# Kernel tuning notes

Measured on AMD Instinct MI355X. Metric: run time of the kernel, lower is better.

The kernel has to match this reference:

```python
import jax, jax.numpy as jnp
import numpy as np

B, N, DPOS, F, P, K = 32, 1024, 3, 64, 128, 16


def setup_inputs() -> dict:
    key = jax.random.key(0)
    kp, kf, kw1, kw2 = jax.random.split(key, 4)
    points = jax.random.normal(kp, (B, N, DPOS), dtype=jnp.float32)
    features = jax.random.normal(kf, (B, N, F), dtype=jnp.float32)
    W1 = jax.random.normal(kw1, (2 * F, 2 * P), dtype=jnp.float32) * (1.0 / np.sqrt(2 * F))
    b1 = jnp.zeros((2 * P,), dtype=jnp.float32)
    W2 = jax.random.normal(kw2, (2 * P, P), dtype=jnp.float32) * (1.0 / np.sqrt(2 * P))
    b2 = jnp.zeros((P,), dtype=jnp.float32)
    return {"points": points, "features": features, "W1": W1, "b1": b1, "W2": W2, "b2": b2}


def reference(points, features, W1, b1, W2, b2):
    # pairwise squared distances: r_i - 2 p_i.p_j + r_j + 1e-5  -> [B, N, N]
    r = jnp.sum(points * points, axis=2, keepdims=True)
    m = jnp.einsum('bnd,bmd->bnm', points, points)
    D = r - 2.0 * m + jnp.swapaxes(r, 1, 2) + 1e-5
    # K+1 nearest (incl. self), drop self -> indices [B, N, K]
    _, idx = jax.lax.top_k(-D, K + 1)
    idx = idx[:, :, 1:]
    # gather neighbor features: [B, N, K, F]
    neighbors = features[jnp.arange(B)[:, None, None], idx]
    center = jnp.broadcast_to(features[:, :, None, :], neighbors.shape)
    local = jnp.concatenate([neighbors - center, center], axis=-1)  # [B,N,K,2F]
    # 2-layer MLP with exact GELU
    h = jax.nn.gelu(jnp.einsum('bnkf,fh->bnkh', local, W1) + b1, approximate=False)
    out = jax.nn.gelu(jnp.einsum('bnkh,hp->bnkp', h, W2) + b2, approximate=False)
    # mean over neighbors -> [B, N, P]
    return jnp.mean(out, axis=2)
```

## Files before the change

kernel.cpp:

```cpp
#include <hip/hip_runtime.h>
#include <math.h>

#define BB 32
#define NN 1024
#define FF 64
#define PP 128
#define KNN 16
#define H2 256
#define F2 128
#define KSEL 17
#define SVCAP 272

typedef float f32x4 __attribute__((ext_vector_type(4)));
typedef _Float16 f16x8 __attribute__((ext_vector_type(8)));

#define GC1 0.39616247f
#define GC3 -0.05891477f
#define GC5 0.00563735f
#define GC7 -2.10439e-4f
#define GXC 3.2988f

__device__ __forceinline__ float gelu_poly(float x) {
    float xc = __builtin_amdgcn_fmed3f(x, -GXC, GXC);
    float s = xc * xc;
    float t = fmaf(s, GC7, GC5);
    t = fmaf(s, t, GC3);
    t = fmaf(s, t, GC1);
    float u = fmaf(xc, t, 0.5f);
    return x * u;
}

__device__ __forceinline__ f16x8 splat8(float f) {
    _Float16 h = (_Float16)f;
    f16x8 v = {h, h, h, h, h, h, h, h};
    return v;
}

__device__ __forceinline__ f16x8 act8(f16x8 gv, f16x8 qv) {
    const f16x8 XL = splat8(-GXC), XH = splat8(GXC);
    const f16x8 C1 = splat8(GC1), C3 = splat8(GC3), C5 = splat8(GC5), C7 = splat8(GC7);
    const f16x8 HF = splat8(0.5f);
    f16x8 x  = gv + qv;
    f16x8 xc = __builtin_elementwise_min(__builtin_elementwise_max(x, XL), XH);
    f16x8 s  = xc * xc;
    f16x8 t  = s * C7 + C5;
    t = s * t + C3;
    t = s * t + C1;
    f16x8 u = xc * t + HF;
    return x * u;
}

__global__ __launch_bounds__(512) void prep_weights(const float* __restrict__ W1,
                                                    const float* __restrict__ W2,
                                                    _Float16* __restrict__ Wcf,
                                                    _Float16* __restrict__ W2f) {
    int tid = blockIdx.x * 512 + threadIdx.x;
    if (tid < 4096) {
        const int lane = tid & 63, quad = lane >> 4, l16 = lane & 15;
        const int kk = (tid >> 6) & 1, n_tile = tid >> 7;
        const int n = n_tile * 16 + l16;
        const int kb = kk * 32 + quad * 8;
        f16x8 v;
#pragma unroll
        for (int j = 0; j < 8; ++j) {
            const int k = kb + j;
            float x = (n < 256) ? W1[k * 256 + n]
                                : (W1[(64 + k) * 256 + (n - 256)] - W1[k * 256 + (n - 256)]);
            v[j] = (_Float16)x;
        }
        *(f16x8*)(Wcf + (size_t)tid * 8) = v;
    } else {
        const int t2 = tid - 4096;
        const int lane = t2 & 63, quad = lane >> 4, l16 = lane & 15;
        const int nt = (t2 >> 6) & 7, kk8 = t2 >> 9;
        const int p = nt * 16 + l16;
        const int hb = kk8 * 32 + quad * 8;
        f16x8 v;
#pragma unroll
        for (int j = 0; j < 8; ++j) v[j] = (_Float16)W2[(size_t)(hb + j) * PP + p];
        *(f16x8*)(W2f + (size_t)t2 * 8) = v;
    }
}

__global__ __launch_bounds__(512, 8) void knn_gq(const float* __restrict__ points,
                                                 int* __restrict__ idx_out,
                                                 const float* __restrict__ feat,
                                                 const _Float16* __restrict__ Wcf,
                                                 const float* __restrict__ b1,
                                                 _Float16* __restrict__ Gall,
                                                 _Float16* __restrict__ Qall) {
    __shared__ __align__(16) unsigned char smem[35840];
    const int t = threadIdx.x;

    if (blockIdx.x >= 4096) {
        _Float16 (*st)[16][136] = (_Float16(*)[16][136])smem;
        const int w8 = t >> 6, lane = t & 63;
        const int w4 = w8 & 3;
        const int quad = lane >> 4, l16 = lane & 15;
        const int gb = blockIdx.x - 4096;
        const int m0 = gb * 32 + (w8 >> 2) * 16;

        f16x8 a[2];
#pragma unroll
        for (int kk = 0; kk < 2; ++kk) {
            const float* ap = feat + (size_t)(m0 + l16) * 64 + kk * 32 + quad * 8;
            float4 a0 = *(const float4*)ap, a1 = *(const float4*)(ap + 4);
            f16x8 v;
            v[0] = (_Float16)a0.x; v[1] = (_Float16)a0.y; v[2] = (_Float16)a0.z; v[3] = (_Float16)a0.w;
            v[4] = (_Float16)a1.x; v[5] = (_Float16)a1.y; v[6] = (_Float16)a1.z; v[7] = (_Float16)a1.w;
            a[kk] = v;
        }
        f32x4 acc[8];
#pragma unroll
        for (int nt = 0; nt < 8; ++nt) acc[nt] = (f32x4){0.f, 0.f, 0.f, 0.f};
#pragma unroll
        for (int kk = 0; kk < 2; ++kk)
#pragma unroll
            for (int nt = 0; nt < 8; ++nt) {
                f16x8 bf = *(const f16x8*)(Wcf + (size_t)(((w4 * 8 + nt) * 2 + kk) * 64 + lane) * 8);
                acc[nt] = __builtin_amdgcn_mfma_f32_16x16x32_f16(a[kk], bf, acc[nt], 0, 0, 0);
            }

        const bool isQ = (w4 >= 2);
#pragma unroll
        for (int nt = 0; nt < 8; ++nt) {
            const int col = nt * 16 + l16;
            const float bias = isQ ? b1[(w4 - 2) * 128 + col] : 0.f;
#pragma unroll
            for (int r = 0; r < 4; ++r)
                st[w8][quad * 4 + r][col] = (_Float16)(acc[nt][r] + bias);
        }
        __syncthreads();

        const int row = lane >> 2, c = lane & 3;
        const int m = m0 + row;
#pragma unroll
        for (int i = 0; i < 4; ++i) {
            const int col = c * 32 + i * 8;
            f16x8 v = *(const f16x8*)&st[w8][row][col];
            if (!isQ) *(f16x8*)(Gall + (size_t)m * H2 + w4 * 128 + col) = v;
            else      *(f16x8*)(Qall + (size_t)m * H2 + (w4 - 2) * 128 + col) = v;
        }
        return;
    }

    float* px = (float*)smem;
    float* py = px + NN;
    float* pz = py + NN;
    float* rr = pz + NN;
    unsigned (*sv_val)[SVCAP] = (unsigned(*)[SVCAP])(smem + 16384);
    unsigned (*sv_idx)[SVCAP] = (unsigned(*)[SVCAP])(smem + 25088);
    unsigned (*tie_idx)[64]   = (unsigned(*)[64])(smem + 33792);

    const int w = t >> 6, lane = t & 63;
    const int b = blockIdx.x >> 7;
    const int q0 = (blockIdx.x & 127) * 8;
    const float* pb = points + (size_t)b * NN * 3;
    const unsigned long long lt = (1ull << lane) - 1ull;

    for (int i = t; i < NN; i += 512) {
        float x = pb[3 * i], y = pb[3 * i + 1], z = pb[3 * i + 2];
        px[i] = x; py[i] = y; pz[i] = z;
        rr[i] = __fadd_rn(__fadd_rn(__fmul_rn(x, x), __fmul_rn(y, y)), __fmul_rn(z, z));
    }
    __syncthreads();

    const int qn = q0 + w;
    const int gq = b * NN + qn;
    const float qx = px[qn], qy = py[qn], qz = pz[qn], qw = rr[qn];

    float D[16];
#pragma unroll
    for (int j = 0; j < 16; ++j) {
        const int m = j * 64 + lane;
        float dot = __fadd_rn(__fadd_rn(__fmul_rn(qx, px[m]), __fmul_rn(qy, py[m])),
                              __fmul_rn(qz, pz[m]));
        D[j] = __fadd_rn(__fadd_rn(__fsub_rn(qw, __fmul_rn(2.0f, dot)), rr[m]), 1e-5f);
    }

    float mnf = D[0];
#pragma unroll
    for (int j = 1; j < 16; ++j) mnf = fminf(mnf, D[j]);
    const unsigned mbits = __float_as_uint(mnf);

    const unsigned mhi = mbits >> 16;
    unsigned Thi = 0;
#pragma unroll
    for (int bit = 15; bit >= 0; --bit) {
        unsigned cand = Thi | (1u << bit);
        int cnt = __popcll(__ballot(mhi < cand));
        if (cnt < KSEL) Thi = cand;
    }
    const unsigned T = (Thi << 16) | 0xFFFFu;

    unsigned base = 0;
#pragma unroll
    for (int j = 0; j < 16; ++j) {
        unsigned vb = __float_as_uint(D[j]);
        bool keep = (vb <= T);
        unsigned long long m = __ballot(keep);
        if (keep) {
            unsigned pos = base + (unsigned)__popcll(m & lt);
            if (pos < SVCAP) { sv_val[w][pos] = vb; sv_idx[w][pos] = j * 64 + lane; }
        }
        base += (unsigned)__popcll(m);
    }
    unsigned C = base > SVCAP ? SVCAP : base;
    const int S = (int)((C + 63) >> 6);

    unsigned Ts = 0;
    if (S == 1) {
        unsigned xv0 = (lane < (int)C) ? sv_val[w][lane] : 0xFFFFFFFFu;
#pragma unroll
        for (int bit = 31; bit >= 0; --bit) {
            unsigned cand = Ts | (1u << bit);
            int cnt = __popcll(__ballot(xv0 < cand));
            if (cnt < KSEL) Ts = cand;
        }
    } else {
        for (int bit = 31; bit >= 0; --bit) {
            unsigned cand = Ts | (1u << bit);
            int cnt = 0;
            for (int s = 0; s < S; ++s) {
                int i = s * 64 + lane;
                unsigned vb = (i < (int)C) ? sv_val[w][i] : 0xFFFFFFFFu;
                cnt += __popcll(__ballot(vb < cand));
            }
            if (cnt < KSEL) Ts = cand;
        }
    }

    int L = 0;
    for (int s = 0; s < S; ++s) {
        int i = s * 64 + lane;
        unsigned vb = (i < (int)C) ? sv_val[w][i] : 0xFFFFFFFFu;
        L += __popcll(__ballot(vb < Ts));
    }
    const int need = KSEL - L;

    unsigned vmin_l = 0xFFFFFFFFu;
    for (int s = 0; s < S; ++s) {
        int i = s * 64 + lane;
        unsigned vb = (i < (int)C) ? sv_val[w][i] : 0xFFFFFFFFu;
        vmin_l = vmin_l < vb ? vmin_l : vb;
    }
#pragma unroll
    for (int off = 32; off >= 1; off >>= 1) {
        unsigned o2 = __shfl_xor(vmin_l, off, 64);
        vmin_l = vmin_l < o2 ? vmin_l : o2;
    }
    const unsigned Vmin = vmin_l;
    unsigned imin_l = 0xFFFFFFFFu;
    for (int s = 0; s < S; ++s) {
        int i = s * 64 + lane;
        unsigned vb = (i < (int)C) ? sv_val[w][i] : 0xFFFFFFFFu;
        unsigned mi = (i < (int)C) ? sv_idx[w][i] : 0xFFFFFFFFu;
        if (vb == Vmin && mi < imin_l) imin_l = mi;
    }
#pragma unroll
    for (int off = 32; off >= 1; off >>= 1) {
        unsigned o2 = __shfl_xor(imin_l, off, 64);
        imin_l = imin_l < o2 ? imin_l : o2;
    }
    const unsigned dropIdx = imin_l;

    int* o = idx_out + (size_t)gq * KNN;
    unsigned wbase = 0, tbase = 0;
    for (int s = 0; s < S; ++s) {
        int i = s * 64 + lane;
        unsigned vb = (i < (int)C) ? sv_val[w][i] : 0xFFFFFFFFu;
        unsigned mi = (i < (int)C) ? sv_idx[w][i] : 0xFFFFFFFFu;
        bool wk = (vb < Ts) && (mi != dropIdx);
        unsigned long long wm = __ballot(wk);
        if (wk) o[wbase + (unsigned)__popcll(wm & lt)] = (int)mi;
        wbase += (unsigned)__popcll(wm);
        bool tk = (vb == Ts);
        unsigned long long tm2 = __ballot(tk);
        if (tk) {
            unsigned tp = tbase + (unsigned)__popcll(tm2 & lt);
            if (tp < 64) tie_idx[w][tp] = mi;
        }
        tbase += (unsigned)__popcll(tm2);
    }
    unsigned tc = tbase > 64 ? 64 : tbase;
    if ((int)tc == need) {
        bool tk = (lane < (int)tc);
        unsigned mi2 = tk ? tie_idx[w][lane] : 0xFFFFFFFFu;
        tk = tk && (mi2 != dropIdx);
        unsigned long long m3 = __ballot(tk);
        if (tk) o[wbase + (unsigned)__popcll(m3 & lt)] = (int)mi2;
    } else if (lane == 0) {
        unsigned pos = wbase;
        for (int r = 0; r < need; ++r) {
            unsigned best = 0xFFFFFFFFu; int bj = 0;
            for (int j2 = 0; j2 < (int)tc; ++j2) {
                unsigned mi = tie_idx[w][j2];
                if (mi < best) { best = mi; bj = j2; }
            }
            tie_idx[w][bj] = 0xFFFFFFFFu;
            if (best != dropIdx) o[pos++] = (int)best;
        }
    }
}

__global__ __launch_bounds__(512, 4) void fused_mlp11(const _Float16* __restrict__ Gall,
                                                      const _Float16* __restrict__ Qall,
                                                      const int* __restrict__ knn_idx,
                                                      const _Float16* __restrict__ W2f,
                                                      const float* __restrict__ b2,
                                                      float* __restrict__ out) {
    __shared__ __align__(16) _Float16 w2s[32768];
    const int t = threadIdx.x, w = t >> 6, lane = t & 63;
    const int quad = lane >> 4, l16 = lane & 15;

    const int lb = ((blockIdx.x & 7) << 8) | (blockIdx.x >> 3);

    const int q0 = lb * 16 + w * 2;
    const int b = q0 >> 10;
    const int nb0 = knn_idx[q0 * KNN + l16];
    const int nb1 = knn_idx[(q0 + 1) * KNN + l16];
    const _Float16* g0 = Gall + ((size_t)(b << 10) + nb0) * H2;
    const _Float16* g1 = Gall + ((size_t)(b << 10) + nb1) * H2;
    const _Float16* qq0 = Qall + (size_t)q0 * H2;
    const _Float16* qq1 = qq0 + H2;

#pragma unroll
    for (int i = 0; i < 8; ++i) {
        f16x8 v = *(const f16x8*)(W2f + (size_t)(i * 4096 + t * 8));
        *(f16x8*)&w2s[i * 4096 + t * 8] = v;
    }

    f32x4 acc[2][8];
#pragma unroll
    for (int tm = 0; tm < 2; ++tm)
#pragma unroll
        for (int nt = 0; nt < 8; ++nt) acc[tm][nt] = (f32x4){0.f, 0.f, 0.f, 0.f};

    __syncthreads();

#pragma unroll
    for (int rk = 0; rk < 8; ++rk) {
        const int ho = rk * 32 + quad * 8;
        f16x8 gA = *(const f16x8*)(g0 + ho);
        f16x8 qA = *(const f16x8*)(qq0 + ho);
        f16x8 gB = *(const f16x8*)(g1 + ho);
        f16x8 qB = *(const f16x8*)(qq1 + ho);
        f16x8 a0 = act8(gA, qA);
        f16x8 a1 = act8(gB, qB);
        const _Float16* bb = &w2s[rk * 4096 + lane * 8];
#pragma unroll
        for (int nt = 0; nt < 8; ++nt) {
            f16x8 bf = *(const f16x8*)(bb + nt * 512);
            acc[0][nt] = __builtin_amdgcn_mfma_f32_16x16x32_f16(a0, bf, acc[0][nt], 0, 0, 0);
            acc[1][nt] = __builtin_amdgcn_mfma_f32_16x16x32_f16(a1, bf, acc[1][nt], 0, 0, 0);
        }
    }

    __syncthreads();
    float* obuf = (float*)w2s;
#pragma unroll
    for (int tm = 0; tm < 2; ++tm)
#pragma unroll
        for (int nt = 0; nt < 8; ++nt) {
            const float bias = b2[nt * 16 + l16];
            float s = 0.f;
#pragma unroll
            for (int r = 0; r < 4; ++r) s += gelu_poly(acc[tm][nt][r] + bias);
            s += __shfl_xor(s, 16, 64);
            s += __shfl_xor(s, 32, 64);
            if (quad == 0)
                obuf[(w * 2 + tm) * 128 + nt * 16 + l16] = s * 0.0625f;
        }
    __syncthreads();
    {
        float4 v = *(const float4*)&obuf[t * 4];
        *(float4*)(out + (size_t)lb * 2048 + t * 4) = v;
    }
}

extern "C" void kernel_launch(void* const* d_in, const int* in_sizes, int n_in,
                              void* d_out, int out_size, void* d_ws, size_t ws_size,
                              hipStream_t stream) {
    const float* points   = (const float*)d_in[0];
    const float* features = (const float*)d_in[1];
    const float* W1 = (const float*)d_in[2];
    const float* b1 = (const float*)d_in[3];
    const float* W2 = (const float*)d_in[4];
    const float* b2 = (const float*)d_in[5];
    float* out = (float*)d_out;

    const size_t IDX_B  = (size_t)BB * NN * KNN * 4;
    const size_t WCF_B  = 512 * 64 * 2;
    const size_t W2F_B  = 256 * 128 * 2;
    const size_t G_B    = (size_t)BB * NN * H2 * 2;

    int* knn_idx = (int*)d_ws;
    char* p = (char*)d_ws + IDX_B;
    _Float16* Wcf  = (_Float16*)p;  p += WCF_B;
    _Float16* W2f  = (_Float16*)p;  p += W2F_B;
    _Float16* Gall = (_Float16*)p;  p += G_B;
    _Float16* Qall = (_Float16*)p;

    prep_weights<<<16, 512, 0, stream>>>(W1, W2, Wcf, W2f);
    knn_gq<<<5120, 512, 0, stream>>>(points, knn_idx, features, Wcf, b1, Gall, Qall);
    fused_mlp11<<<2048, 512, 0, stream>>>(Gall, Qall, knn_idx, W2f, b2, out);
}
```

Before: 190.8 us.

## Use packed fp16 final GELU, interleave point SoA to float2, relax launch bounds

```diff
diff --git a/kernel.cpp b/kernel.cpp
--- a/kernel.cpp
+++ b/kernel.cpp
@@ -13,6 +13,8 @@
 
 typedef float f32x4 __attribute__((ext_vector_type(4)));
 typedef _Float16 f16x8 __attribute__((ext_vector_type(8)));
+typedef _Float16 f16x4 __attribute__((ext_vector_type(4)));
+typedef _Float16 f16x2 __attribute__((ext_vector_type(2)));
 
 #define GC1 0.39616247f
 #define GC3 -0.05891477f
@@ -20,19 +22,14 @@
 #define GC7 -2.10439e-4f
 #define GXC 3.2988f
 
-__device__ __forceinline__ float gelu_poly(float x) {
-    float xc = __builtin_amdgcn_fmed3f(x, -GXC, GXC);
-    float s = xc * xc;
-    float t = fmaf(s, GC7, GC5);
-    t = fmaf(s, t, GC3);
-    t = fmaf(s, t, GC1);
-    float u = fmaf(xc, t, 0.5f);
-    return x * u;
-}
-
 __device__ __forceinline__ f16x8 splat8(float f) {
     _Float16 h = (_Float16)f;
     f16x8 v = {h, h, h, h, h, h, h, h};
+    return v;
+}
+__device__ __forceinline__ f16x4 splat4(float f) {
+    _Float16 h = (_Float16)f;
+    f16x4 v = {h, h, h, h};
     return v;
 }
 
@@ -50,6 +47,26 @@
     return x * u;
 }
 
+__device__ __forceinline__ float gelu4_sum(f32x4 a, float bias) {
+    f16x4 x;
+    x[0] = (_Float16)(a[0] + bias);
+    x[1] = (_Float16)(a[1] + bias);
+    x[2] = (_Float16)(a[2] + bias);
+    x[3] = (_Float16)(a[3] + bias);
+    const f16x4 XL = splat4(-GXC), XH = splat4(GXC);
+    const f16x4 C1 = splat4(GC1), C3 = splat4(GC3), C5 = splat4(GC5), C7 = splat4(GC7);
+    const f16x4 HF = splat4(0.5f);
+    f16x4 xc = __builtin_elementwise_min(__builtin_elementwise_max(x, XL), XH);
+    f16x4 s  = xc * xc;
+    f16x4 t  = s * C7 + C5;
+    t = s * t + C3;
+    t = s * t + C1;
+    f16x4 u = xc * t + HF;
+    f16x4 y = x * u;
+    f16x2 y2 = __builtin_shufflevector(y, y, 0, 1) + __builtin_shufflevector(y, y, 2, 3);
+    return (float)y2[0] + (float)y2[1];
+}
+
 __global__ __launch_bounds__(512) void prep_weights(const float* __restrict__ W1,
                                                     const float* __restrict__ W2,
                                                     _Float16* __restrict__ Wcf,
@@ -144,10 +161,8 @@
         return;
     }
 
-    float* px = (float*)smem;
-    float* py = px + NN;
-    float* pz = py + NN;
-    float* rr = pz + NN;
+    float2* pxy = (float2*)smem;
+    float2* pzr = (float2*)(smem + 8192);
     unsigned (*sv_val)[SVCAP] = (unsigned(*)[SVCAP])(smem + 16384);
     unsigned (*sv_idx)[SVCAP] = (unsigned(*)[SVCAP])(smem + 25088);
     unsigned (*tie_idx)[64]   = (unsigned(*)[64])(smem + 33792);
@@ -160,22 +175,25 @@
 
     for (int i = t; i < NN; i += 512) {
         float x = pb[3 * i], y = pb[3 * i + 1], z = pb[3 * i + 2];
-        px[i] = x; py[i] = y; pz[i] = z;
-        rr[i] = __fadd_rn(__fadd_rn(__fmul_rn(x, x), __fmul_rn(y, y)), __fmul_rn(z, z));
+        float r = __fadd_rn(__fadd_rn(__fmul_rn(x, x), __fmul_rn(y, y)), __fmul_rn(z, z));
+        pxy[i] = make_float2(x, y);
+        pzr[i] = make_float2(z, r);
     }
     __syncthreads();
 
     const int qn = q0 + w;
     const int gq = b * NN + qn;
-    const float qx = px[qn], qy = py[qn], qz = pz[qn], qw = rr[qn];
+    const float2 qv1 = pxy[qn], qv2 = pzr[qn];
+    const float qx = qv1.x, qy = qv1.y, qz = qv2.x, qw = qv2.y;
 
     float D[16];
 #pragma unroll
     for (int j = 0; j < 16; ++j) {
         const int m = j * 64 + lane;
-        float dot = __fadd_rn(__fadd_rn(__fmul_rn(qx, px[m]), __fmul_rn(qy, py[m])),
-                              __fmul_rn(qz, pz[m]));
-        D[j] = __fadd_rn(__fadd_rn(__fsub_rn(qw, __fmul_rn(2.0f, dot)), rr[m]), 1e-5f);
+        const float2 v1 = pxy[m], v2 = pzr[m];
+        float dot = __fadd_rn(__fadd_rn(__fmul_rn(qx, v1.x), __fmul_rn(qy, v1.y)),
+                              __fmul_rn(qz, v2.x));
+        D[j] = __fadd_rn(__fadd_rn(__fsub_rn(qw, __fmul_rn(2.0f, dot)), v2.y), 1e-5f);
     }
 
     float mnf = D[0];
@@ -303,7 +321,7 @@
     }
 }
 
-__global__ __launch_bounds__(512, 4) void fused_mlp11(const _Float16* __restrict__ Gall,
+__global__ __launch_bounds__(512, 3) void fused_mlp12(const _Float16* __restrict__ Gall,
                                                       const _Float16* __restrict__ Qall,
                                                       const int* __restrict__ knn_idx,
                                                       const _Float16* __restrict__ W2f,
@@ -363,9 +381,7 @@
 #pragma unroll
         for (int nt = 0; nt < 8; ++nt) {
             const float bias = b2[nt * 16 + l16];
-            float s = 0.f;
-#pragma unroll
-            for (int r = 0; r < 4; ++r) s += gelu_poly(acc[tm][nt][r] + bias);
+            float s = gelu4_sum(acc[tm][nt], bias);
             s += __shfl_xor(s, 16, 64);
             s += __shfl_xor(s, 32, 64);
             if (quad == 0)
@@ -403,5 +419,5 @@
 
     prep_weights<<<16, 512, 0, stream>>>(W1, W2, Wcf, W2f);
     knn_gq<<<5120, 512, 0, stream>>>(points, knn_idx, features, Wcf, b1, Gall, Qall);
-    fused_mlp11<<<2048, 512, 0, stream>>>(Gall, Qall, knn_idx, W2f, b2, out);
-}
+    fused_mlp12<<<2048, 512, 0, stream>>>(Gall, Qall, knn_idx, W2f, b2, out);
+}
```

Result: no change. 188.7 us (-1.1%).
